# Kernel tuning notes

Hardware: AMD Instinct MI355X
Metric: run time of the kernel (lower is better)

Reference implementation:

```python
import jax, jax.numpy as jnp
import numpy as np

N = 100000      # nodes
E = 1600000     # edges (avg degree 16)
D_IN = 128
D_OUT = 128
ORDER = 2
EPS = 1e-9


def setup_inputs() -> dict:
    key = jax.random.key(0)
    ks = jax.random.split(key, 8)
    inp = {}
    inp["vecs"] = jax.random.normal(ks[0], (N, D_IN), dtype=jnp.float32)
    inp["adj_vals"] = jax.random.uniform(ks[1], (E,), dtype=jnp.float32)
    inp["row"] = jax.random.randint(ks[2], (E,), 0, N)
    inp["col"] = jax.random.randint(ks[3], (E,), 0, N)
    lim = float(np.sqrt(6.0 / (D_IN + D_OUT)))  # glorot uniform
    for o in range(ORDER + 1):
        inp[f"W{o}"] = jax.random.uniform(ks[4 + o], (D_IN, D_OUT), dtype=jnp.float32, minval=-lim, maxval=lim)
        inp[f"b{o}"] = jnp.zeros((D_OUT,), jnp.float32)
        inp[f"off{o}"] = jnp.zeros((1, D_OUT), jnp.float32)
        inp[f"sc{o}"] = jnp.ones((1, D_OUT), jnp.float32)
    return inp


def _spmm(vals, row, col, x):
    # sparse_tensor_dense_matmul: out[r] = sum_e vals[e] * x[col[e]] for row[e]==r
    return jax.ops.segment_sum(vals[:, None] * x[col], row, num_segments=N)


def _f_nonlinear(v, W, b, off, sc):
    vw = jax.nn.relu(v @ W + b)
    mean = jnp.mean(vw, axis=1, keepdims=True)
    var = jnp.var(vw, axis=1, keepdims=True)
    # tf.nn.batch_normalization with per-row moments, eps=1e-9
    return sc * (vw - mean) * jax.lax.rsqrt(var + EPS) + off


def reference(vecs, adj_vals, row, col,
              W0, W1, W2, b0, b1, b2,
              off0, off1, off2, sc0, sc1, sc2):
    Ws = [W0, W1, W2]
    bs = [b0, b1, b2]
    offs = [off0, off1, off2]
    scs = [sc0, sc1, sc2]
    # vecs_hop[k] = A^k @ vecs (dropout=0 -> identity)
    hops = [vecs]
    for _ in range(ORDER):
        hops.append(_spmm(adj_vals, row, col, hops[-1]))
    outs = [_f_nonlinear(hops[o], Ws[o], bs[o], offs[o], scs[o]) for o in range(ORDER + 1)]
    ret = outs[0]
    for o in range(1, ORDER + 1):  # aggr == 'mean' (actually a sum in the source)
        ret = ret + outs[o]
    return ret
```

## Files before the change

### kernel.cpp

```cpp
#include <hip/hip_runtime.h>
#include <math.h>

#define NN 100000
#define DD 128
#define NB 391
#define RP_PAD 100004

typedef short bf16x8 __attribute__((ext_vector_type(8)));
typedef float f32x4  __attribute__((ext_vector_type(4)));
typedef unsigned uint4v __attribute__((ext_vector_type(4)));

__device__ __forceinline__ unsigned f2bf_rne(float f) {
    unsigned u = __float_as_uint(f);
    return (u + 0x7FFFu + ((u >> 16) & 1u)) >> 16;
}
__device__ __forceinline__ unsigned packbf(float a, float b) {
    return f2bf_rne(a) | (f2bf_rne(b) << 16);
}
__device__ __forceinline__ float bf_lo(unsigned u) { return __uint_as_float(u << 16); }
__device__ __forceinline__ float bf_hi(unsigned u) { return __uint_as_float(u & 0xFFFF0000u); }

__device__ __forceinline__ int2 ldnt_edge(const int2* p) {
    long long v = __builtin_nontemporal_load((const long long*)p);
    int2 r;
    r.x = (int)(v & 0xffffffffll);
    r.y = (int)(((unsigned long long)v) >> 32);
    return r;
}

__global__ __launch_bounds__(1024) void bucket_scatter(
    const int* __restrict__ row, const int* __restrict__ col,
    const float* __restrict__ vals, int* __restrict__ bcnt,
    int2* __restrict__ ep_raw, int E, int CAP)
{
    __shared__ int cnt[NB];
    __shared__ int base[NB];
    const int t = threadIdx.x;
    if (t < NB) cnt[t] = 0;
    __syncthreads();
    const int cb = blockIdx.x * 8192;
    const int ce = min(cb + 8192, E);

    int   rr[8];
    int   cc[8];
    float vv[8];
    #pragma unroll
    for (int i = 0; i < 8; i++) {
        int j = cb + t + i * 1024;
        bool ok = j < ce;
        rr[i] = -1;
        if (ok) {
            rr[i] = row[j];
            cc[i] = __builtin_nontemporal_load(col + j);
            vv[i] = __builtin_nontemporal_load(vals + j);
            atomicAdd(&cnt[rr[i] >> 8], 1);
        }
    }
    __syncthreads();
    if (t < NB) {
        int c = cnt[t];
        base[t] = c ? (t * CAP + atomicAdd(&bcnt[t], c)) : 0;
        cnt[t] = 0;
    }
    __syncthreads();
    #pragma unroll
    for (int i = 0; i < 8; i++) {
        int r = rr[i];
        if (r >= 0) {
            int b = r >> 8;
            int off = atomicAdd(&cnt[b], 1);
            unsigned meta = (unsigned)cc[i] | ((unsigned)(r & 255) << 17);
            ep_raw[base[b] + off] = make_int2((int)meta, __float_as_int(vv[i]));
        }
    }
}

__global__ __launch_bounds__(256) void csr_finish_convert(
    const int* __restrict__ bcnt, const int2* __restrict__ ep_raw,
    int* __restrict__ row_ptr, int2* __restrict__ ep,
    const float* __restrict__ vecs, unsigned short* __restrict__ vecs_bf,
    const float* __restrict__ W0, const float* __restrict__ W1,
    const float* __restrict__ W2, unsigned short* __restrict__ Wt,
    int CAP, int N, int E, int n8)
{
    const int b = blockIdx.x;
    const int t = threadIdx.x;

    if (b >= NB) {
        if (b < NB + 24) {
            const int b2 = b - NB;
            const float* W = (b2 < 8) ? W0 : ((b2 < 16) ? W1 : W2);
            unsigned short* dst = Wt + (b2 >> 3) * DD * DD;
            int idx = (b2 & 7) * 256 + t;
            int n = idx >> 4;
            int kc = (idx & 15) * 8;
            unsigned r[4];
            #pragma unroll
            for (int j = 0; j < 4; j++) {
                float a = W[(kc + 2 * j) * DD + n];
                float c = W[(kc + 2 * j + 1) * DD + n];
                r[j] = packbf(a, c);
            }
            *(uint4*)(dst + n * DD + kc) = make_uint4(r[0], r[1], r[2], r[3]);
        } else {
            int i = (b - NB - 24) * 256 + t;
            if (i >= n8) return;
            f32x4 a = __builtin_nontemporal_load((const f32x4*)vecs + (size_t)i * 2);
            f32x4 c = __builtin_nontemporal_load((const f32x4*)vecs + (size_t)i * 2 + 1);
            uint4v o;
            o.x = packbf(a.x, a.y); o.y = packbf(a.z, a.w);
            o.z = packbf(c.x, c.y); o.w = packbf(c.z, c.w);
            ((uint4v*)vecs_bf)[i] = o;
        }
        return;
    }

    __shared__ int red[256];
    __shared__ int rcnt[256];
    __shared__ int rcur[256];
    __shared__ int wsum[4];

    int part = 0;
    for (int j = t; j < b; j += 256) part += bcnt[j];
    red[t] = part;
    __syncthreads();
    #pragma unroll
    for (int off = 128; off > 0; off >>= 1) {
        if (t < off) red[t] += red[t + off];
        __syncthreads();
    }
    const int dst = red[0];
    const int cnt = bcnt[b];
    const int src = b * CAP;

    rcnt[t] = 0;
    __syncthreads();
    for (int j = t; j < cnt; j += 256)
        atomicAdd(&rcnt[(unsigned)ep_raw[src + j].x >> 17], 1);
    __syncthreads();

    int v = rcnt[t];
    int lane = t & 63;
    int inc = v;
    #pragma unroll
    for (int off = 1; off < 64; off <<= 1) {
        int u = __shfl_up(inc, off, 64);
        if (lane >= off) inc += u;
    }
    if (lane == 63) wsum[t >> 6] = inc;
    __syncthreads();
    int woff = 0;
    for (int i = 0; i < (t >> 6); i++) woff += wsum[i];
    int excl = woff + inc - v;

    int grow = b * 256 + t;
    if (grow < N) row_ptr[grow] = dst + excl;
    rcur[t] = excl;
    __syncthreads();

    for (int j = t; j < cnt; j += 256) {
        int2 rec = ldnt_edge(ep_raw + src + j);
        unsigned meta = (unsigned)rec.x;
        int rlo = meta >> 17;
        int c = (int)(meta & 0x1FFFFu);
        int p = atomicAdd(&rcur[rlo], 1);
        ep[dst + p] = make_int2(c, rec.y);
    }
    if (b == 0 && t == 0) row_ptr[N] = E;
}

__device__ __forceinline__ void accum8(float* acc, uint4 u, float v) {
    acc[0] += v * bf_lo(u.x); acc[1] += v * bf_hi(u.x);
    acc[2] += v * bf_lo(u.y); acc[3] += v * bf_hi(u.y);
    acc[4] += v * bf_lo(u.z); acc[5] += v * bf_hi(u.z);
    acc[6] += v * bf_lo(u.w); acc[7] += v * bf_hi(u.w);
}

__global__ __launch_bounds__(256) void spmm_bf16(
    const uint4* __restrict__ x, const int* __restrict__ row_ptr,
    const int2* __restrict__ ep, uint4* __restrict__ out, int N)
{
    int t = blockIdx.x * 256 + threadIdx.x;
    int g = t >> 4;
    int lane = t & 15;
    if (g >= N) return;

    int s = row_ptr[g];
    int e = row_ptr[g + 1];
    float acc[8] = {0.f, 0.f, 0.f, 0.f, 0.f, 0.f, 0.f, 0.f};

    int k = s;
    for (; k + 8 <= e; k += 8) {
        int2 E0 = ep[k + 0], E1 = ep[k + 1], E2 = ep[k + 2], E3 = ep[k + 3];
        int2 E4 = ep[k + 4], E5 = ep[k + 5], E6 = ep[k + 6], E7 = ep[k + 7];
        uint4 X0 = x[(size_t)E0.x * 16 + lane];
        uint4 X1 = x[(size_t)E1.x * 16 + lane];
        uint4 X2 = x[(size_t)E2.x * 16 + lane];
        uint4 X3 = x[(size_t)E3.x * 16 + lane];
        uint4 X4 = x[(size_t)E4.x * 16 + lane];
        uint4 X5 = x[(size_t)E5.x * 16 + lane];
        uint4 X6 = x[(size_t)E6.x * 16 + lane];
        uint4 X7 = x[(size_t)E7.x * 16 + lane];
        accum8(acc, X0, __int_as_float(E0.y));
        accum8(acc, X1, __int_as_float(E1.y));
        accum8(acc, X2, __int_as_float(E2.y));
        accum8(acc, X3, __int_as_float(E3.y));
        accum8(acc, X4, __int_as_float(E4.y));
        accum8(acc, X5, __int_as_float(E5.y));
        accum8(acc, X6, __int_as_float(E6.y));
        accum8(acc, X7, __int_as_float(E7.y));
    }
    for (; k + 4 <= e; k += 4) {
        int2 E0 = ep[k + 0], E1 = ep[k + 1], E2 = ep[k + 2], E3 = ep[k + 3];
        uint4 X0 = x[(size_t)E0.x * 16 + lane];
        uint4 X1 = x[(size_t)E1.x * 16 + lane];
        uint4 X2 = x[(size_t)E2.x * 16 + lane];
        uint4 X3 = x[(size_t)E3.x * 16 + lane];
        accum8(acc, X0, __int_as_float(E0.y));
        accum8(acc, X1, __int_as_float(E1.y));
        accum8(acc, X2, __int_as_float(E2.y));
        accum8(acc, X3, __int_as_float(E3.y));
    }
    for (; k < e; k++) {
        int2 E0 = ep[k];
        uint4 X0 = x[(size_t)E0.x * 16 + lane];
        accum8(acc, X0, __int_as_float(E0.y));
    }

    uint4 o;
    o.x = packbf(acc[0], acc[1]); o.y = packbf(acc[2], acc[3]);
    o.z = packbf(acc[4], acc[5]); o.w = packbf(acc[6], acc[7]);
    out[(size_t)g * 16 + lane] = o;
}

__device__ __forceinline__ void bn_accum(
    f32x4* acc, const float* __restrict__ bias, const float* __restrict__ off,
    const float* __restrict__ sc, int i, float facc[8][4])
{
    float bc[8], sv[8], ov[8];
    #pragma unroll
    for (int ct = 0; ct < 8; ct++) {
        int c = ct * 16 + i;
        bc[ct] = bias[c]; sv[ct] = sc[c]; ov[ct] = off[c];
    }
    float s[4] = {0.f, 0.f, 0.f, 0.f};
    float qq[4] = {0.f, 0.f, 0.f, 0.f};
    #pragma unroll
    for (int ct = 0; ct < 8; ct++) {
        #pragma unroll
        for (int r = 0; r < 4; r++) {
            float v = fmaxf(acc[ct][r] + bc[ct], 0.f);
            acc[ct][r] = v;
            s[r] += v;
            qq[r] += v * v;
        }
    }
    #pragma unroll
    for (int r = 0; r < 4; r++) {
        #pragma unroll
        for (int m = 1; m <= 8; m <<= 1) {
            s[r]  += __shfl_xor(s[r],  m, 64);
            qq[r] += __shfl_xor(qq[r], m, 64);
        }
    }
    #pragma unroll
    for (int r = 0; r < 4; r++) {
        float mn = s[r] * 0.0078125f;
        float var = qq[r] * 0.0078125f - mn * mn;
        float rs = rsqrtf(var + 1e-9f);
        #pragma unroll
        for (int ct = 0; ct < 8; ct++)
            facc[ct][r] += sv[ct] * (acc[ct][r] - mn) * rs + ov[ct];
    }
}

__global__ __launch_bounds__(256) void fused_dense_mfma(
    const unsigned short* __restrict__ h0,
    const unsigned short* __restrict__ h1,
    const unsigned short* __restrict__ h2,
    const unsigned short* __restrict__ Wt,
    const float* __restrict__ b0, const float* __restrict__ b1,
    const float* __restrict__ b2,
    const float* __restrict__ off0, const float* __restrict__ off1,
    const float* __restrict__ off2,
    const float* __restrict__ sc0, const float* __restrict__ sc1,
    const float* __restrict__ sc2,
    float* __restrict__ out, int N)
{
    __shared__ uint4 Bl[2048];

    const int tid  = threadIdx.x;
    const int wave = tid >> 6;
    const int lane = tid & 63;
    const int i    = lane & 15;
    const int q    = lane >> 4;
    const int slab = blockIdx.x * 64 + wave * 16;

    int arow = slab + i;
    if (arow >= N) arow = N - 1;

    const unsigned short* hops[3] = {h0, h1, h2};
    const float* bs[3]  = {b0, b1, b2};
    const float* ofs[3] = {off0, off1, off2};
    const float* scs[3] = {sc0, sc1, sc2};
    const bf16x8* Bv = (const bf16x8*)Bl;

    float facc[8][4];
    #pragma unroll
    for (int ct = 0; ct < 8; ct++)
        #pragma unroll
        for (int r = 0; r < 4; r++) facc[ct][r] = 0.f;

    for (int o = 0; o < 3; o++) {
        const uint4* Wg = (const uint4*)(Wt + o * DD * DD);
        #pragma unroll
        for (int j = 0; j < 8; j++) {
            int c  = j * 256 + tid;
            int nn = c & 127;
            int kc = c >> 7;
            Bl[kc * 128 + nn] = Wg[nn * 16 + kc];
        }
        __syncthreads();

        const unsigned short* arow_p = hops[o] + (size_t)arow * DD + q * 8;
        f32x4 acc[8];
        #pragma unroll
        for (int ct = 0; ct < 8; ct++) acc[ct] = (f32x4){0.f, 0.f, 0.f, 0.f};
        #pragma unroll
        for (int kb = 0; kb < 4; kb++) {
            bf16x8 a = __builtin_nontemporal_load((const bf16x8*)(arow_p + kb * 32));
            const int kc = kb * 4 + q;
            #pragma unroll
            for (int ct = 0; ct < 8; ct++) {
                bf16x8 b = Bv[kc * 128 + ct * 16 + i];
                acc[ct] = __builtin_amdgcn_mfma_f32_16x16x32_bf16(a, b, acc[ct], 0, 0, 0);
            }
        }
        bn_accum(acc, bs[o], ofs[o], scs[o], i, facc);
        __syncthreads();
    }

    #pragma unroll
    for (int r = 0; r < 4; r++) {
        int orow = slab + q * 4 + r;
        if (orow < N) {
            float* op = out + (size_t)orow * DD + i;
            #pragma unroll
            for (int ct = 0; ct < 8; ct++)
                __builtin_nontemporal_store(facc[ct][r], op + ct * 16);
        }
    }
}

extern "C" void kernel_launch(void* const* d_in, const int* in_sizes, int n_in,
                              void* d_out, int out_size, void* d_ws, size_t ws_size,
                              hipStream_t stream)
{
    const float* vecs = (const float*)d_in[0];
    const float* adj  = (const float*)d_in[1];
    const int*   row  = (const int*)d_in[2];
    const int*   col  = (const int*)d_in[3];
    const float* W0   = (const float*)d_in[4];
    const float* b0   = (const float*)d_in[5];
    const float* off0 = (const float*)d_in[6];
    const float* sc0  = (const float*)d_in[7];
    const float* W1   = (const float*)d_in[8];
    const float* b1   = (const float*)d_in[9];
    const float* off1 = (const float*)d_in[10];
    const float* sc1  = (const float*)d_in[11];
    const float* W2   = (const float*)d_in[12];
    const float* b2   = (const float*)d_in[13];
    const float* off2 = (const float*)d_in[14];
    const float* sc2  = (const float*)d_in[15];

    const int E = in_sizes[1];
    const int N = NN;

    const int avg = (E + NB - 1) / NB;
    const int CAP = (avg + 8 * (int)sqrt((double)avg) + 79) & ~15;

    unsigned short* hop1_bf = (unsigned short*)d_ws;
    unsigned short* hop2_bf = hop1_bf + (size_t)N * DD;
    unsigned short* vecs_bf = hop2_bf + (size_t)N * DD;
    unsigned short* Wt_bf   = vecs_bf + (size_t)N * DD;
    int*   row_ptr  = (int*)(Wt_bf + 3 * DD * DD);
    int*   bcnt     = row_ptr + RP_PAD;
    int2*  ep_raw   = (int2*)(bcnt + 512);
    int2*  epack    = ep_raw + (size_t)NB * CAP;

    hipMemsetAsync(bcnt, 0, NB * sizeof(int), stream);

    const int cb = (E + 8191) / 8192;
    bucket_scatter<<<cb, 1024, 0, stream>>>(row, col, adj, bcnt, ep_raw, E, CAP);

    const int n8 = N * DD / 8;
    const int vb = (n8 + 255) / 256;
    csr_finish_convert<<<NB + 24 + vb, 256, 0, stream>>>(
        bcnt, ep_raw, row_ptr, epack,
        vecs, vecs_bf, W0, W1, W2, Wt_bf,
        CAP, N, E, n8);

    int sb = (N * 16 + 255) / 256;
    spmm_bf16<<<sb, 256, 0, stream>>>(
        (const uint4*)vecs_bf, row_ptr, epack, (uint4*)hop1_bf, N);
    spmm_bf16<<<sb, 256, 0, stream>>>(
        (const uint4*)hop1_bf, row_ptr, epack, (uint4*)hop2_bf, N);

    const int db = (N + 63) / 64;
    fused_dense_mfma<<<db, 256, 0, stream>>>(
        vecs_bf, hop1_bf, hop2_bf, Wt_bf,
        b0, b1, b2, off0, off1, off2, sc0, sc1, sc2,
        (float*)d_out, N);
}
```

Baseline: 336.3 us.

## Fuse second SpMM hop into dense MFMA kernel via shared-memory tile

```diff
diff --git a/kernel.cpp b/kernel.cpp
--- a/kernel.cpp
+++ b/kernel.cpp
@@ -176,19 +176,11 @@
     acc[6] += v * bf_lo(u.w); acc[7] += v * bf_hi(u.w);
 }
 
-__global__ __launch_bounds__(256) void spmm_bf16(
-    const uint4* __restrict__ x, const int* __restrict__ row_ptr,
-    const int2* __restrict__ ep, uint4* __restrict__ out, int N)
-{
-    int t = blockIdx.x * 256 + threadIdx.x;
-    int g = t >> 4;
-    int lane = t & 15;
-    if (g >= N) return;
-
-    int s = row_ptr[g];
-    int e = row_ptr[g + 1];
+__device__ __forceinline__ uint4 row_gather(
+    const uint4* __restrict__ x, const int2* __restrict__ ep,
+    int s, int e, int lane)
+{
     float acc[8] = {0.f, 0.f, 0.f, 0.f, 0.f, 0.f, 0.f, 0.f};
-
     int k = s;
     for (; k + 8 <= e; k += 8) {
         int2 E0 = ep[k + 0], E1 = ep[k + 1], E2 = ep[k + 2], E3 = ep[k + 3];
@@ -226,11 +218,22 @@
         uint4 X0 = x[(size_t)E0.x * 16 + lane];
         accum8(acc, X0, __int_as_float(E0.y));
     }
-
     uint4 o;
     o.x = packbf(acc[0], acc[1]); o.y = packbf(acc[2], acc[3]);
     o.z = packbf(acc[4], acc[5]); o.w = packbf(acc[6], acc[7]);
-    out[(size_t)g * 16 + lane] = o;
+    return o;
+}
+
+__global__ __launch_bounds__(256) void spmm_bf16(
+    const uint4* __restrict__ x, const int* __restrict__ row_ptr,
+    const int2* __restrict__ ep, uint4* __restrict__ out, int N)
+{
+    int t = blockIdx.x * 256 + threadIdx.x;
+    int g = t >> 4;
+    int lane = t & 15;
+    if (g >= N) return;
+    out[(size_t)g * 16 + lane] =
+        row_gather(x, ep, row_ptr[g], row_ptr[g + 1], lane);
 }
 
 __device__ __forceinline__ void bn_accum(
@@ -274,10 +277,10 @@
     }
 }
 
-__global__ __launch_bounds__(256) void fused_dense_mfma(
+__global__ __launch_bounds__(256) void fused_spmm_dense(
     const unsigned short* __restrict__ h0,
     const unsigned short* __restrict__ h1,
-    const unsigned short* __restrict__ h2,
+    const int* __restrict__ row_ptr, const int2* __restrict__ ep,
     const unsigned short* __restrict__ Wt,
     const float* __restrict__ b0, const float* __restrict__ b1,
     const float* __restrict__ b2,
@@ -288,22 +291,42 @@
     float* __restrict__ out, int N)
 {
     __shared__ uint4 Bl[2048];
+    __shared__ uint4 Ht[1024];
 
     const int tid  = threadIdx.x;
     const int wave = tid >> 6;
     const int lane = tid & 63;
     const int i    = lane & 15;
     const int q    = lane >> 4;
-    const int slab = blockIdx.x * 64 + wave * 16;
+    const int sbase = blockIdx.x * 64;
+    const int slab  = sbase + wave * 16;
+
+    {
+        const int grp = tid >> 4;
+        const int ln  = tid & 15;
+        #pragma unroll
+        for (int it = 0; it < 4; it++) {
+            int gl = it * 16 + grp;
+            int g  = sbase + gl;
+            if (g < N) {
+                uint4 o = row_gather((const uint4*)h1, ep,
+                                     row_ptr[g], row_ptr[g + 1], ln);
+                Ht[gl * 16 + (ln ^ (gl & 15))] = o;
+            }
+        }
+    }
+    __syncthreads();
 
     int arow = slab + i;
     if (arow >= N) arow = N - 1;
-
-    const unsigned short* hops[3] = {h0, h1, h2};
+    const int hloc = arow - sbase;
+
+    const unsigned short* hops[2] = {h0, h1};
     const float* bs[3]  = {b0, b1, b2};
     const float* ofs[3] = {off0, off1, off2};
     const float* scs[3] = {sc0, sc1, sc2};
-    const bf16x8* Bv = (const bf16x8*)Bl;
+    const bf16x8* Bv  = (const bf16x8*)Bl;
+    const bf16x8* Hv  = (const bf16x8*)Ht;
 
     float facc[8][4];
     #pragma unroll
@@ -322,18 +345,32 @@
         }
         __syncthreads();
 
-        const unsigned short* arow_p = hops[o] + (size_t)arow * DD + q * 8;
         f32x4 acc[8];
         #pragma unroll
         for (int ct = 0; ct < 8; ct++) acc[ct] = (f32x4){0.f, 0.f, 0.f, 0.f};
-        #pragma unroll
-        for (int kb = 0; kb < 4; kb++) {
-            bf16x8 a = __builtin_nontemporal_load((const bf16x8*)(arow_p + kb * 32));
-            const int kc = kb * 4 + q;
+
+        if (o < 2) {
+            const unsigned short* arow_p = hops[o] + (size_t)arow * DD + q * 8;
             #pragma unroll
-            for (int ct = 0; ct < 8; ct++) {
-                bf16x8 b = Bv[kc * 128 + ct * 16 + i];
-                acc[ct] = __builtin_amdgcn_mfma_f32_16x16x32_bf16(a, b, acc[ct], 0, 0, 0);
+            for (int kb = 0; kb < 4; kb++) {
+                bf16x8 a = __builtin_nontemporal_load((const bf16x8*)(arow_p + kb * 32));
+                const int kc = kb * 4 + q;
+                #pragma unroll
+                for (int ct = 0; ct < 8; ct++) {
+                    bf16x8 b = Bv[kc * 128 + ct * 16 + i];
+                    acc[ct] = __builtin_amdgcn_mfma_f32_16x16x32_bf16(a, b, acc[ct], 0, 0, 0);
+                }
+            }
+        } else {
+            #pragma unroll
+            for (int kb = 0; kb < 4; kb++) {
+                bf16x8 a = Hv[hloc * 16 + ((kb * 4 + q) ^ (hloc & 15))];
+                const int kc = kb * 4 + q;
+                #pragma unroll
+                for (int ct = 0; ct < 8; ct++) {
+                    bf16x8 b = Bv[kc * 128 + ct * 16 + i];
+                    acc[ct] = __builtin_amdgcn_mfma_f32_16x16x32_bf16(a, b, acc[ct], 0, 0, 0);
+                }
             }
         }
         bn_accum(acc, bs[o], ofs[o], scs[o], i, facc);
@@ -380,8 +417,7 @@
     const int CAP = (avg + 8 * (int)sqrt((double)avg) + 79) & ~15;
 
     unsigned short* hop1_bf = (unsigned short*)d_ws;
-    unsigned short* hop2_bf = hop1_bf + (size_t)N * DD;
-    unsigned short* vecs_bf = hop2_bf + (size_t)N * DD;
+    unsigned short* vecs_bf = hop1_bf + (size_t)N * DD;
     unsigned short* Wt_bf   = vecs_bf + (size_t)N * DD;
     int*   row_ptr  = (int*)(Wt_bf + 3 * DD * DD);
     int*   bcnt     = row_ptr + RP_PAD;
@@ -403,12 +439,10 @@
     int sb = (N * 16 + 255) / 256;
     spmm_bf16<<<sb, 256, 0, stream>>>(
         (const uint4*)vecs_bf, row_ptr, epack, (uint4*)hop1_bf, N);
-    spmm_bf16<<<sb, 256, 0, stream>>>(
-        (const uint4*)hop1_bf, row_ptr, epack, (uint4*)hop2_bf, N);
 
     const int db = (N + 63) / 64;
-    fused_dense_mfma<<<db, 256, 0, stream>>>(
-        vecs_bf, hop1_bf, hop2_bf, Wt_bf,
+    fused_spmm_dense<<<db, 256, 0, stream>>>(
+        vecs_bf, hop1_bf, row_ptr, epack, Wt_bf,
         b0, b1, b2, off0, off1, off2, sc0, sc1, sc2,
         (float*)d_out, N);
 }
```

After: 366.2 us. 8.9% more time.
